# Kernel optimization log

Hardware: AMD Instinct MI355X
Metric: run time of the kernel (lower is better)

## Reference

```python
import math
import jax, jax.numpy as jnp
import numpy as np

EMBED_DIM = 1024
NUM_HEADS = 16
HEAD_DIM = EMBED_DIM // NUM_HEADS  # 64


def setup_inputs() -> dict:
    key = jax.random.key(0)
    kx, kq, ko = jax.random.split(key, 3)
    B, S, D = 4, 1024, EMBED_DIM
    x = jax.random.normal(kx, (B, S, D), dtype=jnp.float32)
    # xavier_uniform for Dense kernels, zeros for biases
    def xavier(k, shape):
        fan_in, fan_out = shape[0], shape[1]
        limit = math.sqrt(6.0 / (fan_in + fan_out))
        return jax.random.uniform(k, shape, jnp.float32, -limit, limit)
    W_qkv = xavier(kq, (D, 3 * D))
    b_qkv = jnp.zeros((3 * D,), jnp.float32)
    W_o = xavier(ko, (D, D))
    b_o = jnp.zeros((D,), jnp.float32)
    return {"x": x, "W_qkv": W_qkv, "b_qkv": b_qkv, "W_o": W_o, "b_o": b_o}


def reference(x, W_qkv, b_qkv, W_o, b_o):
    B, S, D = x.shape
    H, hd = NUM_HEADS, HEAD_DIM
    qkv = x @ W_qkv + b_qkv                         # [B,S,3D]
    qkv = qkv.reshape(B, S, H, 3 * hd).transpose(0, 2, 1, 3)  # [B,H,S,3hd]
    q, k, v = jnp.split(qkv, 3, axis=-1)            # each [B,H,S,hd]
    attn_logits = jnp.einsum('bhqd,bhkd->bhqk', q, k) / math.sqrt(hd)
    attention = jax.nn.softmax(attn_logits, axis=-1)  # [B,H,S,S]
    values = jnp.einsum('bhqk,bhkd->bhqd', attention, v)
    values = values.transpose(0, 2, 1, 3).reshape(B, S, D)
    o = values @ W_o + b_o
    return (o, attention)
```

## Files before the change

### kernel.cpp

```cpp
#include <hip/hip_runtime.h>

#define B_   4
#define S_   1024
#define D_   1024
#define H_   16
#define HD_  64

typedef __bf16 bf16_t;
typedef __attribute__((ext_vector_type(8))) __bf16 bf16x8;
typedef __attribute__((ext_vector_type(4))) float f32x4;

#define MFMA16(a, b, c) __builtin_amdgcn_mfma_f32_16x16x32_bf16((a), (b), (c), 0, 0, 0)

__device__ inline unsigned short f2bf(float f) {
    unsigned int u = __builtin_bit_cast(unsigned int, f);
    u += 0x7FFFu + ((u >> 16) & 1u);
    return (unsigned short)(u >> 16);
}

__device__ inline bf16x8 ld_frag(const unsigned short* p) {
    uint4 u = *(const uint4*)p;
    return __builtin_bit_cast(bf16x8, u);
}

__device__ inline void gload_lds16(const unsigned short* g, unsigned short* l) {
    __builtin_amdgcn_global_load_lds(
        (const __attribute__((address_space(1))) void*)g,
        (__attribute__((address_space(3))) void*)l,
        16, 0, 0);
}

__global__ __launch_bounds__(256) void convert_f32_bf16(
    const float* __restrict__ in, unsigned short* __restrict__ out)
{
    const size_t idx = (size_t)blockIdx.x * 256 + threadIdx.x;
    float4 v = *(const float4*)(in + idx * 4);
    unsigned short* o = out + idx * 4;
    ushort4 r;
    r.x = f2bf(v.x); r.y = f2bf(v.y); r.z = f2bf(v.z); r.w = f2bf(v.w);
    *(ushort4*)o = r;
}

__global__ __launch_bounds__(256) void transpose_f32_bf16(
    const float* __restrict__ in, unsigned short* __restrict__ out,
    int K, int N)
{
    __shared__ float T[64][65];
    const int tid = threadIdx.x;
    const int k0 = blockIdx.y * 64, n0 = blockIdx.x * 64;
#pragma unroll
    for (int i = 0; i < 4; ++i) {
        int c = tid + i * 256;
        int row = c >> 4, col = (c & 15) << 2;
        float4 v = *(const float4*)(in + (size_t)(k0 + row) * N + n0 + col);
        T[row][col + 0] = v.x; T[row][col + 1] = v.y;
        T[row][col + 2] = v.z; T[row][col + 3] = v.w;
    }
    __syncthreads();
#pragma unroll
    for (int i = 0; i < 4; ++i) {
        int c = tid + i * 256;
        int nr = c >> 4, kc = (c & 15) << 2;
        ushort4 r;
        r.x = f2bf(T[kc + 0][nr]); r.y = f2bf(T[kc + 1][nr]);
        r.z = f2bf(T[kc + 2][nr]); r.w = f2bf(T[kc + 3][nr]);
        *(ushort4*)(out + (size_t)(n0 + nr) * K + k0 + kc) = r;
    }
}

__global__ __launch_bounds__(256) void transpose_v_bf16(
    const unsigned short* __restrict__ v,
    unsigned short* __restrict__ vt)
{
    __shared__ unsigned short T[64][65];
    const int tid = threadIdx.x;
    const int kt = blockIdx.x, bh = blockIdx.y;
    const int b = bh >> 4, h = bh & 15;
#pragma unroll
    for (int i = 0; i < 2; ++i) {
        const int c = tid + i * 256;
        const int key = c >> 3, off = (c & 7) << 3;
        uint4 u = *(const uint4*)(v + (size_t)(b * 1024 + kt * 64 + key) * 1024 + h * 64 + off);
        union { uint4 u4; unsigned short us[8]; } uu; uu.u4 = u;
#pragma unroll
        for (int t = 0; t < 8; ++t) T[key][off + t] = uu.us[t];
    }
    __syncthreads();
#pragma unroll
    for (int i = 0; i < 16; ++i) {
        const int c = tid + i * 256;
        const int dim = c >> 6, key = c & 63;
        vt[((size_t)bh * 64 + dim) * 1024 + kt * 64 + key] = T[key][dim];
    }
}

template<int MODE>
__global__ __launch_bounds__(256) void gemm_bf16(
    const unsigned short* __restrict__ A,
    const unsigned short* __restrict__ Bt,
    const float* __restrict__ bias,
    unsigned short* __restrict__ qk,
    unsigned short* __restrict__ vnat,
    float* __restrict__ out,
    int K, int N)
{
    __shared__ unsigned short Alds[128][64];
    __shared__ unsigned short Blds[128][64];
    const int tid  = threadIdx.x;
    const int l    = tid & 63, w = tid >> 6;
    const int wm   = w >> 1, wn = w & 1;
    const int quad = l >> 4, n16 = l & 15;
    const int bm = blockIdx.y * 128, bn = blockIdx.x * 128;

    const int lrow = l >> 3;
    const int lcol = (l & 7) << 3;

    const f32x4 zero4 = {0.f, 0.f, 0.f, 0.f};
    f32x4 acc[4][4];
#pragma unroll
    for (int i = 0; i < 4; ++i)
#pragma unroll
        for (int j = 0; j < 4; ++j) acc[i][j] = zero4;

    for (int k0 = 0; k0 < K; k0 += 64) {
#pragma unroll
        for (int i = 0; i < 4; ++i) {
            const int c8  = (w * 4 + i) * 8;
            const int row = c8 + lrow;
            gload_lds16(A  + (size_t)(bm + row) * K + k0 + lcol, &Alds[c8][0]);
            gload_lds16(Bt + (size_t)(bn + row) * K + k0 + lcol, &Blds[c8][0]);
        }
        __syncthreads();
#pragma unroll
        for (int kk = 0; kk < 2; ++kk) {
            const int kc = kk * 32 + quad * 8;
            bf16x8 af[4], bfv[4];
#pragma unroll
            for (int i = 0; i < 4; ++i) af[i]  = ld_frag(&Alds[wm * 64 + i * 16 + n16][kc]);
#pragma unroll
            for (int j = 0; j < 4; ++j) bfv[j] = ld_frag(&Blds[wn * 64 + j * 16 + n16][kc]);
#pragma unroll
            for (int i = 0; i < 4; ++i)
#pragma unroll
                for (int j = 0; j < 4; ++j)
                    acc[i][j] = MFMA16(af[i], bfv[j], acc[i][j]);
        }
        __syncthreads();
    }

#pragma unroll
    for (int j = 0; j < 4; ++j) {
        const int col0 = bn + wn * 64 + j * 16;
        const int col  = col0 + n16;
        const float bv = bias ? bias[col] : 0.f;
        if (MODE == 0) {
            const int head = col0 / 192;
            const int rem  = col0 % 192;
            if (rem < 128) {
#pragma unroll
                for (int i = 0; i < 4; ++i)
#pragma unroll
                    for (int r = 0; r < 4; ++r) {
                        int row = bm + wm * 64 + i * 16 + quad * 4 + r;
                        qk[(size_t)row * 2048 + head * 128 + rem + n16] =
                            f2bf(acc[i][j][r] + bv);
                    }
            } else {
                const int dcol = head * 64 + (rem - 128) + n16;
#pragma unroll
                for (int i = 0; i < 4; ++i)
#pragma unroll
                    for (int r = 0; r < 4; ++r) {
                        int row = bm + wm * 64 + i * 16 + quad * 4 + r;
                        vnat[(size_t)row * 1024 + dcol] = f2bf(acc[i][j][r] + bv);
                    }
            }
        } else {
#pragma unroll
            for (int i = 0; i < 4; ++i)
#pragma unroll
                for (int r = 0; r < 4; ++r) {
                    int row = bm + wm * 64 + i * 16 + quad * 4 + r;
                    out[(size_t)row * N + col] = acc[i][j][r] + bv;
                }
        }
    }
}

__global__ __launch_bounds__(256) void attn_fused(
    const unsigned short* __restrict__ qk,
    const unsigned short* __restrict__ vt,
    float* __restrict__ attn,
    unsigned short* __restrict__ values)
{
    __shared__ unsigned short KV[2][64][72];
    __shared__ unsigned short Plds[16][1032];
    __shared__ float redbuf[2][4][16];

    const int qb = blockIdx.x, bh = blockIdx.y;
    const int b = bh >> 4, h = bh & 15;
    const int tid = threadIdx.x, l = tid & 63, w = tid >> 6;
    const int quad = l >> 4, n16 = l & 15;

    const int skey = tid >> 3;
    const int soff = (tid & 7) << 3;

    bf16x8 qf[2];
    {
        const unsigned short* qbase =
            qk + (size_t)(b * 1024 + qb * 16 + n16) * 2048 + h * 128 + quad * 8;
        qf[0] = ld_frag(qbase);
        qf[1] = ld_frag(qbase + 32);
    }

    const f32x4 zero4 = {0.f, 0.f, 0.f, 0.f};
    f32x4 c[16];
#pragma unroll
    for (int s = 0; s < 16; ++s) c[s] = zero4;

    const unsigned short* kbase = qk + (size_t)(b * 1024) * 2048 + h * 128 + 64;
#pragma unroll
    for (int i = 0; i < 2; ++i)
        *(uint4*)&KV[0][skey + i * 32][soff] =
            *(const uint4*)(kbase + (size_t)(skey + i * 32) * 2048 + soff);
    __syncthreads();
    for (int s = 0; s < 16; ++s) {
        if (s < 15) {
#pragma unroll
            for (int i = 0; i < 2; ++i)
                *(uint4*)&KV[(s + 1) & 1][skey + i * 32][soff] =
                    *(const uint4*)(kbase +
                        (size_t)((s + 1) * 64 + skey + i * 32) * 2048 + soff);
        }
        const int p = s & 1;
        const int krow = w * 16 + n16;
        bf16x8 k0f = ld_frag(&KV[p][krow][quad * 8]);
        bf16x8 k1f = ld_frag(&KV[p][krow][32 + quad * 8]);
        c[s] = MFMA16(qf[0], k0f, c[s]);
        c[s] = MFMA16(qf[1], k1f, c[s]);
        __syncthreads();
    }

    float mx[4] = {-1e30f, -1e30f, -1e30f, -1e30f};
#pragma unroll
    for (int s = 0; s < 16; ++s)
#pragma unroll
        for (int r = 0; r < 4; ++r) {
            c[s][r] *= 0.125f;
            mx[r] = fmaxf(mx[r], c[s][r]);
        }
#pragma unroll
    for (int off = 1; off <= 8; off <<= 1)
#pragma unroll
        for (int r = 0; r < 4; ++r)
            mx[r] = fmaxf(mx[r], __shfl_xor(mx[r], off, 64));
    if (n16 == 0)
#pragma unroll
        for (int r = 0; r < 4; ++r) redbuf[0][w][quad * 4 + r] = mx[r];
    __syncthreads();
#pragma unroll
    for (int r = 0; r < 4; ++r) {
        const int row = quad * 4 + r;
        float m = redbuf[0][0][row];
        m = fmaxf(m, redbuf[0][1][row]);
        m = fmaxf(m, redbuf[0][2][row]);
        m = fmaxf(m, redbuf[0][3][row]);
        mx[r] = m;
    }

    float sm[4] = {0.f, 0.f, 0.f, 0.f};
#pragma unroll
    for (int s = 0; s < 16; ++s)
#pragma unroll
        for (int r = 0; r < 4; ++r) {
            float e = __expf(c[s][r] - mx[r]);
            c[s][r] = e;
            sm[r] += e;
        }
#pragma unroll
    for (int off = 1; off <= 8; off <<= 1)
#pragma unroll
        for (int r = 0; r < 4; ++r)
            sm[r] += __shfl_xor(sm[r], off, 64);
    if (n16 == 0)
#pragma unroll
        for (int r = 0; r < 4; ++r) redbuf[1][w][quad * 4 + r] = sm[r];
    __syncthreads();
    float inv[4];
#pragma unroll
    for (int r = 0; r < 4; ++r) {
        const int row = quad * 4 + r;
        inv[r] = 1.f / (redbuf[1][0][row] + redbuf[1][1][row] +
                        redbuf[1][2][row] + redbuf[1][3][row]);
    }

    float* abase = attn + ((size_t)bh * 1024 + qb * 16) * 1024;
#pragma unroll
    for (int s = 0; s < 16; ++s)
#pragma unroll
        for (int r = 0; r < 4; ++r) {
            const float a = c[s][r] * inv[r];
            const int row = quad * 4 + r;
            const int key = s * 64 + w * 16 + n16;
            abase[(size_t)row * 1024 + key] = a;
            Plds[row][key] = f2bf(a);
        }

    f32x4 o = zero4;
    const unsigned short* vbase = vt + (size_t)bh * 65536;
#pragma unroll
    for (int i = 0; i < 2; ++i)
        *(uint4*)&KV[0][skey + i * 32][soff] =
            *(const uint4*)(vbase + (size_t)(skey + i * 32) * 1024 + soff);
    __syncthreads();
    for (int s = 0; s < 16; ++s) {
        if (s < 15) {
#pragma unroll
            for (int i = 0; i < 2; ++i)
                *(uint4*)&KV[(s + 1) & 1][skey + i * 32][soff] =
                    *(const uint4*)(vbase +
                        (size_t)(skey + i * 32) * 1024 + (s + 1) * 64 + soff);
        }
        const int p = s & 1;
#pragma unroll
        for (int kk = 0; kk < 2; ++kk) {
            bf16x8 pf = ld_frag(&Plds[n16][s * 64 + kk * 32 + quad * 8]);
            bf16x8 vf = ld_frag(&KV[p][w * 16 + n16][kk * 32 + quad * 8]);
            o = MFMA16(pf, vf, o);
        }
        __syncthreads();
    }

#pragma unroll
    for (int r = 0; r < 4; ++r) {
        const int row = quad * 4 + r;
        values[(size_t)(b * 1024 + qb * 16 + row) * 1024 + h * 64 + w * 16 + n16] =
            f2bf(o[r]);
    }
}

extern "C" void kernel_launch(void* const* d_in, const int* in_sizes, int n_in,
                              void* d_out, int out_size, void* d_ws, size_t ws_size,
                              hipStream_t stream)
{
    const float* x     = (const float*)d_in[0];
    const float* W_qkv = (const float*)d_in[1];
    const float* b_qkv = (const float*)d_in[2];
    const float* W_o   = (const float*)d_in[3];
    const float* b_o   = (const float*)d_in[4];

    float* o_out    = (float*)d_out;
    float* attn_out = o_out + (size_t)B_ * S_ * D_;

    const size_t M1 = 1ull << 20;
    unsigned short* ws      = (unsigned short*)d_ws;
    unsigned short* x_bf    = ws;
    unsigned short* wqkvt   = ws + 4 * M1;
    unsigned short* wot     = ws + 7 * M1;
    unsigned short* qkbuf   = ws + 8 * M1;
    unsigned short* vtbuf   = ws + 16 * M1;
    unsigned short* valbuf  = ws + 20 * M1;

    convert_f32_bf16<<<4096, 256, 0, stream>>>(x, x_bf);
    transpose_f32_bf16<<<dim3(3072 / 64, 1024 / 64), 256, 0, stream>>>(W_qkv, wqkvt, 1024, 3072);
    transpose_f32_bf16<<<dim3(1024 / 64, 1024 / 64), 256, 0, stream>>>(W_o, wot, 1024, 1024);

    gemm_bf16<0><<<dim3(3072 / 128, 4096 / 128), 256, 0, stream>>>(
        x_bf, wqkvt, b_qkv, qkbuf, valbuf, nullptr, 1024, 3072);

    transpose_v_bf16<<<dim3(S_ / 64, B_ * H_), 256, 0, stream>>>(valbuf, vtbuf);

    attn_fused<<<dim3(S_ / 16, B_ * H_), 256, 0, stream>>>(
        qkbuf, vtbuf, attn_out, valbuf);

    gemm_bf16<1><<<dim3(1024 / 128, 4096 / 128), 256, 0, stream>>>(
        valbuf, wot, b_o, nullptr, nullptr, o_out, 1024, 1024);
}
```

Before: 486.9 us.

## Load K/V fragments directly from global and fold softmax scale into Q

Removes the double-buffered LDS staging of K and V tiles in the attention kernel. Each lane now loads its MFMA fragments straight from global memory, which drops the per-iteration barriers and the LDS traffic. The 1/sqrt(hd) scale moves into the QKV GEMM epilogue, so Q is stored pre-scaled and the per-element multiply on the logits goes away. An explicit barrier is added after P is written to LDS. Direct loads use strided 16-byte accesses per lane that may coalesce less well, and both loops are now fully unrolled, which raises register pressure.

```diff
diff --git a/kernel.cpp b/kernel.cpp
--- a/kernel.cpp
+++ b/kernel.cpp
@@ -157,13 +157,14 @@
             const int head = col0 / 192;
             const int rem  = col0 % 192;
             if (rem < 128) {
+                const float sc = (rem < 64) ? 0.125f : 1.0f;
 #pragma unroll
                 for (int i = 0; i < 4; ++i)
 #pragma unroll
                     for (int r = 0; r < 4; ++r) {
                         int row = bm + wm * 64 + i * 16 + quad * 4 + r;
                         qk[(size_t)row * 2048 + head * 128 + rem + n16] =
-                            f2bf(acc[i][j][r] + bv);
+                            f2bf((acc[i][j][r] + bv) * sc);
                     }
             } else {
                 const int dcol = head * 64 + (rem - 128) + n16;
@@ -193,7 +194,6 @@
     float* __restrict__ attn,
     unsigned short* __restrict__ values)
 {
-    __shared__ unsigned short KV[2][64][72];
     __shared__ unsigned short Plds[16][1032];
     __shared__ float redbuf[2][4][16];
 
@@ -201,9 +201,6 @@
     const int b = bh >> 4, h = bh & 15;
     const int tid = threadIdx.x, l = tid & 63, w = tid >> 6;
     const int quad = l >> 4, n16 = l & 15;
-
-    const int skey = tid >> 3;
-    const int soff = (tid & 7) << 3;
 
     bf16x8 qf[2];
     {
@@ -220,35 +217,20 @@
 
     const unsigned short* kbase = qk + (size_t)(b * 1024) * 2048 + h * 128 + 64;
 #pragma unroll
-    for (int i = 0; i < 2; ++i)
-        *(uint4*)&KV[0][skey + i * 32][soff] =
-            *(const uint4*)(kbase + (size_t)(skey + i * 32) * 2048 + soff);
-    __syncthreads();
     for (int s = 0; s < 16; ++s) {
-        if (s < 15) {
-#pragma unroll
-            for (int i = 0; i < 2; ++i)
-                *(uint4*)&KV[(s + 1) & 1][skey + i * 32][soff] =
-                    *(const uint4*)(kbase +
-                        (size_t)((s + 1) * 64 + skey + i * 32) * 2048 + soff);
-        }
-        const int p = s & 1;
-        const int krow = w * 16 + n16;
-        bf16x8 k0f = ld_frag(&KV[p][krow][quad * 8]);
-        bf16x8 k1f = ld_frag(&KV[p][krow][32 + quad * 8]);
+        const unsigned short* kr = kbase + (size_t)(s * 64 + w * 16 + n16) * 2048;
+        bf16x8 k0f = ld_frag(kr + quad * 8);
+        bf16x8 k1f = ld_frag(kr + 32 + quad * 8);
         c[s] = MFMA16(qf[0], k0f, c[s]);
         c[s] = MFMA16(qf[1], k1f, c[s]);
-        __syncthreads();
     }
 
     float mx[4] = {-1e30f, -1e30f, -1e30f, -1e30f};
 #pragma unroll
     for (int s = 0; s < 16; ++s)
 #pragma unroll
-        for (int r = 0; r < 4; ++r) {
-            c[s][r] *= 0.125f;
+        for (int r = 0; r < 4; ++r)
             mx[r] = fmaxf(mx[r], c[s][r]);
-        }
 #pragma unroll
     for (int off = 1; off <= 8; off <<= 1)
 #pragma unroll
@@ -305,30 +287,19 @@
             abase[(size_t)row * 1024 + key] = a;
             Plds[row][key] = f2bf(a);
         }
+    __syncthreads();
 
     f32x4 o = zero4;
-    const unsigned short* vbase = vt + (size_t)bh * 65536;
-#pragma unroll
-    for (int i = 0; i < 2; ++i)
-        *(uint4*)&KV[0][skey + i * 32][soff] =
-            *(const uint4*)(vbase + (size_t)(skey + i * 32) * 1024 + soff);
-    __syncthreads();
+    const unsigned short* vbase = vt + (size_t)bh * 65536 +
+                                  (size_t)(w * 16 + n16) * 1024;
+#pragma unroll
     for (int s = 0; s < 16; ++s) {
-        if (s < 15) {
-#pragma unroll
-            for (int i = 0; i < 2; ++i)
-                *(uint4*)&KV[(s + 1) & 1][skey + i * 32][soff] =
-                    *(const uint4*)(vbase +
-                        (size_t)(skey + i * 32) * 1024 + (s + 1) * 64 + soff);
-        }
-        const int p = s & 1;
 #pragma unroll
         for (int kk = 0; kk < 2; ++kk) {
             bf16x8 pf = ld_frag(&Plds[n16][s * 64 + kk * 32 + quad * 8]);
-            bf16x8 vf = ld_frag(&KV[p][w * 16 + n16][kk * 32 + quad * 8]);
+            bf16x8 vf = ld_frag(vbase + s * 64 + kk * 32 + quad * 8);
             o = MFMA16(pf, vf, o);
         }
-        __syncthreads();
     }
 
 #pragma unroll
```

Result: slower. 497.0 us (+2.1%).
